# Kernel tuning notes

Measured on AMD Instinct MI355X. Metric: run time of the kernel, lower is better.

## Reference

```python
import jax, jax.numpy as jnp
import numpy as np

N_NODES = 50000
N_EDGES = 800000
D_NODE = 64
D_EDGE = 64


def setup_inputs() -> dict:
    key = jax.random.key(0)
    ks = jax.random.split(key, 6)
    node_scalars = jax.random.normal(ks[0], (N_NODES, D_NODE), dtype=jnp.float32)
    edge_feats = jax.random.normal(ks[1], (N_EDGES, D_EDGE), dtype=jnp.float32)
    src_idxs = jax.random.randint(ks[2], (N_EDGES,), 0, N_NODES, dtype=jnp.int32)
    dst_idxs = jax.random.randint(ks[3], (N_EDGES,), 0, N_NODES, dtype=jnp.int32)
    in_dim = 2 * D_NODE + D_EDGE  # 192
    # He-ish init for the MLP weights
    W1 = jax.random.normal(ks[4], (in_dim, D_EDGE), dtype=jnp.float32) / np.sqrt(in_dim)
    b1 = jnp.zeros((D_EDGE,), dtype=jnp.float32)
    W2 = jax.random.normal(ks[5], (D_EDGE, D_EDGE), dtype=jnp.float32) / np.sqrt(D_EDGE)
    b2 = jnp.zeros((D_EDGE,), dtype=jnp.float32)
    ln_gamma = jnp.ones((D_EDGE,), dtype=jnp.float32)
    ln_beta = jnp.zeros((D_EDGE,), dtype=jnp.float32)
    return {
        "node_scalars": node_scalars,
        "edge_feats": edge_feats,
        "src_idxs": src_idxs,
        "dst_idxs": dst_idxs,
        "W1": W1,
        "b1": b1,
        "W2": W2,
        "b2": b2,
        "ln_gamma": ln_gamma,
        "ln_beta": ln_beta,
    }


def _layer_norm(x, gamma, beta, eps=1e-5):
    mu = jnp.mean(x, axis=-1, keepdims=True)
    var = jnp.mean(jnp.square(x - mu), axis=-1, keepdims=True)
    return (x - mu) * jax.lax.rsqrt(var + eps) * gamma + beta


def reference(node_scalars, edge_feats, src_idxs, dst_idxs, W1, b1, W2, b2, ln_gamma, ln_beta):
    # gather endpoint node features per edge and concat with edge feats -> [E, 2*Dn + De]
    mlp_in = jnp.concatenate(
        [node_scalars[src_idxs], node_scalars[dst_idxs], edge_feats], axis=-1
    )
    h = jax.nn.silu(mlp_in @ W1 + b1)
    h = jax.nn.silu(h @ W2 + b2)
    return _layer_norm(edge_feats + h, ln_gamma, ln_beta)
```

## Files before the change

kernel.cpp:

```cpp
#include <hip/hip_runtime.h>

#define NE 800000
#define NN 50000
#define D  64
#define K1 192
#define AST 200
#define WSW_ELEMS (K1 * D + D * D)

typedef __bf16 bf16x4v __attribute__((ext_vector_type(4)));
typedef __bf16 bf16x8  __attribute__((ext_vector_type(8)));
typedef float  f32x4   __attribute__((ext_vector_type(4)));

__global__ void prep_all(const float* __restrict__ W1,
                         const float* __restrict__ W2,
                         const float* __restrict__ nodes,
                         __bf16* __restrict__ ws, int do_nodes) {
  const int b = blockIdx.x;
  if (b < 64) {
    int i = b * 256 + threadIdx.x;
    if (i < K1 * D) {
      int k = i >> 6, n = i & 63;
      ws[n * K1 + k] = (__bf16)W1[i];
    } else {
      int j = i - K1 * D;
      int k = j >> 6, n = j & 63;
      ws[K1 * D + n * D + k] = (__bf16)W2[j];
    }
  } else if (do_nodes) {
    __bf16* nb = ws + WSW_ELEMS;
    const int nvec = NN * D / 4;
    for (int v = (b - 64) * 256 + threadIdx.x; v < nvec; v += 2048 * 256) {
      f32x4 x = *(const f32x4*)(nodes + (size_t)v * 4);
      bf16x4v y;
      #pragma unroll
      for (int j = 0; j < 4; ++j) y[j] = (__bf16)x[j];
      *(bf16x4v*)(nb + (size_t)v * 4) = y;
    }
  }
}

__device__ __forceinline__ void wave_lds_fence() {
  __asm__ volatile("s_waitcnt lgkmcnt(0)" ::: "memory");
}

__device__ __forceinline__ float silu(float x) {
  return x * __builtin_amdgcn_rcpf(1.f + __expf(-x));
}

template <int MODE>
__global__ __launch_bounds__(256, 3)
void edge_kernel(const float* __restrict__ nodes, const float* __restrict__ ef,
                 const int* __restrict__ srci, const int* __restrict__ dsti,
                 const float* __restrict__ W1, const float* __restrict__ b1,
                 const float* __restrict__ W2, const float* __restrict__ b2,
                 const float* __restrict__ gmm, const float* __restrict__ bta,
                 const __bf16* __restrict__ wsw, float* __restrict__ out) {
  __shared__ __align__(16) __bf16 w1t[64 * AST];
  __shared__ __align__(16) __bf16 atile_all[4][16 * AST];
  __shared__ float sb1[64], sb2[64], sg[64], sbt[64];

  const int tid = threadIdx.x;
  const int wave = tid >> 6, lane = tid & 63;
  const int quad = lane >> 4, m16 = lane & 15;

  if (MODE >= 1) {
    const uint2* s1 = (const uint2*)wsw;
    for (int c = tid; c < 3072; c += 256) {
      int n = c / 48, kc = c - n * 48;
      *(uint2*)&w1t[n * AST + kc * 4] = s1[c];
    }
  } else {
    for (int i = tid; i < K1 * D; i += 256) {
      int k = i >> 6, n = i & 63;
      w1t[n * AST + k] = (__bf16)W1[i];
    }
  }
  if (tid < 64)       sb1[tid]       = b1[tid];
  else if (tid < 128) sb2[tid - 64]  = b2[tid - 64];
  else if (tid < 192) sg[tid - 128]  = gmm[tid - 128];
  else                sbt[tid - 192] = bta[tid - 192];

  bf16x8 w2f[2][4];
  if (MODE >= 1) {
    const __bf16* w2t = wsw + K1 * D;
    #pragma unroll
    for (int ki = 0; ki < 2; ++ki)
      #pragma unroll
      for (int nt = 0; nt < 4; ++nt)
        w2f[ki][nt] = *(const bf16x8*)&w2t[(nt * 16 + m16) * 64 + ki * 32 + quad * 8];
  } else {
    #pragma unroll
    for (int ki = 0; ki < 2; ++ki)
      #pragma unroll
      for (int nt = 0; nt < 4; ++nt) {
        const int n = nt * 16 + m16;
        #pragma unroll
        for (int j = 0; j < 8; ++j)
          w2f[ki][nt][j] = (__bf16)W2[(ki * 32 + quad * 8 + j) * 64 + n];
      }
  }
  __syncthreads();

  __bf16* At = atile_all[wave];
  float*  Af = (float*)At;

  const __bf16* nb = (MODE == 2) ? (wsw + WSW_ELEMS) : nullptr;

  #pragma unroll 1
  for (int t = 0; t < 4; ++t) {
    const int base = blockIdx.x * 256 + wave * 64 + t * 16;

    int si[4], di[4];
    #pragma unroll
    for (int i = 0; i < 4; ++i) {
      si[i] = srci[base + i * 4 + quad];
      di[i] = dsti[base + i * 4 + quad];
    }
    #pragma unroll
    for (int i = 0; i < 4; ++i) {
      const int row = i * 4 + quad;
      f32x4 ev = *(const f32x4*)(ef + (size_t)(base + row) * D + m16 * 4);
      bf16x4v sb, db, eb;
      if (MODE == 2) {
        sb = *(const bf16x4v*)(nb + (size_t)si[i] * D + m16 * 4);
        db = *(const bf16x4v*)(nb + (size_t)di[i] * D + m16 * 4);
      } else {
        f32x4 sv = *(const f32x4*)(nodes + (size_t)si[i] * D + m16 * 4);
        f32x4 dv = *(const f32x4*)(nodes + (size_t)di[i] * D + m16 * 4);
        #pragma unroll
        for (int j = 0; j < 4; ++j) { sb[j] = (__bf16)sv[j]; db[j] = (__bf16)dv[j]; }
      }
      #pragma unroll
      for (int j = 0; j < 4; ++j) eb[j] = (__bf16)ev[j];
      *(bf16x4v*)&At[row * AST +       m16 * 4] = sb;
      *(bf16x4v*)&At[row * AST +  64 + m16 * 4] = db;
      *(bf16x4v*)&At[row * AST + 128 + m16 * 4] = eb;
    }
    wave_lds_fence();

    f32x4 acc[4] = {};
    #pragma unroll
    for (int ki = 0; ki < 6; ++ki) {
      bf16x8 a = *(const bf16x8*)&At[m16 * AST + ki * 32 + quad * 8];
      #pragma unroll
      for (int nt = 0; nt < 4; ++nt) {
        bf16x8 bfv = *(const bf16x8*)&w1t[(nt * 16 + m16) * AST + ki * 32 + quad * 8];
        acc[nt] = __builtin_amdgcn_mfma_f32_16x16x32_bf16(a, bfv, acc[nt], 0, 0, 0);
      }
    }

    #pragma unroll
    for (int nt = 0; nt < 4; ++nt) {
      const int c = nt * 16 + m16;
      const float bb = sb1[c];
      #pragma unroll
      for (int r = 0; r < 4; ++r)
        At[(quad * 4 + r) * AST + c] = (__bf16)silu(acc[nt][r] + bb);
    }
    wave_lds_fence();

    f32x4 acc2[4] = {};
    #pragma unroll
    for (int ki = 0; ki < 2; ++ki) {
      bf16x8 a = *(const bf16x8*)&At[m16 * AST + ki * 32 + quad * 8];
      #pragma unroll
      for (int nt = 0; nt < 4; ++nt)
        acc2[nt] = __builtin_amdgcn_mfma_f32_16x16x32_bf16(a, w2f[ki][nt], acc2[nt], 0, 0, 0);
    }

    #pragma unroll
    for (int r = 0; r < 4; ++r) {
      const int row = quad * 4 + r;
      float x[4];
      float sum = 0.f;
      #pragma unroll
      for (int nt = 0; nt < 4; ++nt) {
        const int c = nt * 16 + m16;
        float h = silu(acc2[nt][r] + sb2[c]);
        float efv = (float)At[row * AST + 128 + c];
        x[nt] = efv + h;
        sum += x[nt];
      }
      float sq = x[0] * x[0] + x[1] * x[1] + x[2] * x[2] + x[3] * x[3];
      #pragma unroll
      for (int off = 1; off < 16; off <<= 1) {
        sum += __shfl_xor(sum, off);
        sq  += __shfl_xor(sq, off);
      }
      const float mean = sum * (1.f / 64.f);
      const float var  = sq * (1.f / 64.f) - mean * mean;
      const float rstd = rsqrtf(var + 1e-5f);
      #pragma unroll
      for (int nt = 0; nt < 4; ++nt) {
        const int c = nt * 16 + m16;
        Af[row * (AST / 2) + c] = (x[nt] - mean) * rstd * sg[c] + sbt[c];
      }
    }
    wave_lds_fence();

    #pragma unroll
    for (int i = 0; i < 4; ++i) {
      const int row = i * 4 + quad;
      f32x4 ov = *(const f32x4*)&Af[row * (AST / 2) + m16 * 4];
      *(f32x4*)(out + (size_t)(base + row) * D + m16 * 4) = ov;
    }
    wave_lds_fence();
  }
}

extern "C" void kernel_launch(void* const* d_in, const int* in_sizes, int n_in,
                              void* d_out, int out_size, void* d_ws, size_t ws_size,
                              hipStream_t stream) {
  const float* nodes = (const float*)d_in[0];
  const float* ef    = (const float*)d_in[1];
  const int*   srci  = (const int*)d_in[2];
  const int*   dsti  = (const int*)d_in[3];
  const float* W1    = (const float*)d_in[4];
  const float* b1    = (const float*)d_in[5];
  const float* W2    = (const float*)d_in[6];
  const float* b2    = (const float*)d_in[7];
  const float* gmm   = (const float*)d_in[8];
  const float* bta   = (const float*)d_in[9];
  float* out = (float*)d_out;

  const int blocks = NE / 256;
  const size_t WS_W = (size_t)WSW_ELEMS * 2;
  const size_t WS_FULL = WS_W + (size_t)NN * D * 2;

  if (ws_size >= WS_FULL) {
    prep_all<<<64 + 2048, 256, 0, stream>>>(W1, W2, nodes, (__bf16*)d_ws, 1);
    edge_kernel<2><<<blocks, 256, 0, stream>>>(
        nodes, ef, srci, dsti, W1, b1, W2, b2, gmm, bta,
        (const __bf16*)d_ws, out);
  } else if (ws_size >= WS_W) {
    prep_all<<<64, 256, 0, stream>>>(W1, W2, nodes, (__bf16*)d_ws, 0);
    edge_kernel<1><<<blocks, 256, 0, stream>>>(
        nodes, ef, srci, dsti, W1, b1, W2, b2, gmm, bta,
        (const __bf16*)d_ws, out);
  } else {
    edge_kernel<0><<<blocks, 256, 0, stream>>>(
        nodes, ef, srci, dsti, W1, b1, W2, b2, gmm, bta, nullptr, out);
  }
}
```

Baseline: 398.1 us.

## Software-pipeline gathers across tiles and store output directly from registers

Prefetches the next tile's edge indices, node gathers and edge features into registers while the current tile's first GEMM runs, with the loop fully unrolled and sched barriers pinning the loads in place. This aims to hide gather latency behind MFMA work. It also drops the LDS staging of the LayerNorm output and writes scalar floats straight to global memory. That removes an LDS round trip but makes the stores strided 4-byte writes instead of 16-byte vectors. The register prefetch buffers raise register pressure, and occupancy is pinned to exactly 3 waves per EU.

```diff
diff --git a/kernel.cpp b/kernel.cpp
--- a/kernel.cpp
+++ b/kernel.cpp
@@ -48,7 +48,8 @@
 }
 
 template <int MODE>
-__global__ __launch_bounds__(256, 3)
+__global__ __launch_bounds__(256)
+__attribute__((amdgpu_waves_per_eu(3, 3)))
 void edge_kernel(const float* __restrict__ nodes, const float* __restrict__ ef,
                  const int* __restrict__ srci, const int* __restrict__ dsti,
                  const float* __restrict__ W1, const float* __restrict__ b1,
@@ -102,39 +103,60 @@
   __syncthreads();
 
   __bf16* At = atile_all[wave];
-  float*  Af = (float*)At;
 
   const __bf16* nb = (MODE == 2) ? (wsw + WSW_ELEMS) : nullptr;
-
-  #pragma unroll 1
+  const int wbase = blockIdx.x * 256 + wave * 64;
+
+  bf16x4v sb[4], db[4];
+  f32x4 svf[4], dvf[4];
+  f32x4 ev[4];
+  int si[4], di[4];
+
+  #pragma unroll
+  for (int i = 0; i < 4; ++i) {
+    si[i] = srci[wbase + i * 4 + quad];
+    di[i] = dsti[wbase + i * 4 + quad];
+  }
+  #pragma unroll
+  for (int i = 0; i < 4; ++i) {
+    const int row = i * 4 + quad;
+    if (MODE == 2) {
+      sb[i] = *(const bf16x4v*)(nb + (size_t)si[i] * D + m16 * 4);
+      db[i] = *(const bf16x4v*)(nb + (size_t)di[i] * D + m16 * 4);
+    } else {
+      svf[i] = *(const f32x4*)(nodes + (size_t)si[i] * D + m16 * 4);
+      dvf[i] = *(const f32x4*)(nodes + (size_t)di[i] * D + m16 * 4);
+    }
+    ev[i] = *(const f32x4*)(ef + (size_t)(wbase + row) * D + m16 * 4);
+  }
+
+  #pragma unroll
   for (int t = 0; t < 4; ++t) {
-    const int base = blockIdx.x * 256 + wave * 64 + t * 16;
-
-    int si[4], di[4];
-    #pragma unroll
-    for (int i = 0; i < 4; ++i) {
-      si[i] = srci[base + i * 4 + quad];
-      di[i] = dsti[base + i * 4 + quad];
-    }
+    const int base = wbase + t * 16;
+
     #pragma unroll
     for (int i = 0; i < 4; ++i) {
       const int row = i * 4 + quad;
-      f32x4 ev = *(const f32x4*)(ef + (size_t)(base + row) * D + m16 * 4);
-      bf16x4v sb, db, eb;
+      bf16x4v s_, d_, e_;
       if (MODE == 2) {
-        sb = *(const bf16x4v*)(nb + (size_t)si[i] * D + m16 * 4);
-        db = *(const bf16x4v*)(nb + (size_t)di[i] * D + m16 * 4);
+        s_ = sb[i]; d_ = db[i];
       } else {
-        f32x4 sv = *(const f32x4*)(nodes + (size_t)si[i] * D + m16 * 4);
-        f32x4 dv = *(const f32x4*)(nodes + (size_t)di[i] * D + m16 * 4);
         #pragma unroll
-        for (int j = 0; j < 4; ++j) { sb[j] = (__bf16)sv[j]; db[j] = (__bf16)dv[j]; }
-      }
-      #pragma unroll
-      for (int j = 0; j < 4; ++j) eb[j] = (__bf16)ev[j];
-      *(bf16x4v*)&At[row * AST +       m16 * 4] = sb;
-      *(bf16x4v*)&At[row * AST +  64 + m16 * 4] = db;
-      *(bf16x4v*)&At[row * AST + 128 + m16 * 4] = eb;
+        for (int j = 0; j < 4; ++j) { s_[j] = (__bf16)svf[i][j]; d_[j] = (__bf16)dvf[i][j]; }
+      }
+      #pragma unroll
+      for (int j = 0; j < 4; ++j) e_[j] = (__bf16)ev[i][j];
+      *(bf16x4v*)&At[row * AST +       m16 * 4] = s_;
+      *(bf16x4v*)&At[row * AST +  64 + m16 * 4] = d_;
+      *(bf16x4v*)&At[row * AST + 128 + m16 * 4] = e_;
+    }
+
+    if (t < 3) {
+      #pragma unroll
+      for (int i = 0; i < 4; ++i) {
+        si[i] = srci[base + 16 + i * 4 + quad];
+        di[i] = dsti[base + 16 + i * 4 + quad];
+      }
     }
     wave_lds_fence();
 
@@ -147,6 +169,23 @@
         bf16x8 bfv = *(const bf16x8*)&w1t[(nt * 16 + m16) * AST + ki * 32 + quad * 8];
         acc[nt] = __builtin_amdgcn_mfma_f32_16x16x32_bf16(a, bfv, acc[nt], 0, 0, 0);
       }
+    }
+
+    if (t < 3) {
+      __builtin_amdgcn_sched_barrier(0);
+      #pragma unroll
+      for (int i = 0; i < 4; ++i) {
+        const int row = i * 4 + quad;
+        if (MODE == 2) {
+          sb[i] = *(const bf16x4v*)(nb + (size_t)si[i] * D + m16 * 4);
+          db[i] = *(const bf16x4v*)(nb + (size_t)di[i] * D + m16 * 4);
+        } else {
+          svf[i] = *(const f32x4*)(nodes + (size_t)si[i] * D + m16 * 4);
+          dvf[i] = *(const f32x4*)(nodes + (size_t)di[i] * D + m16 * 4);
+        }
+        ev[i] = *(const f32x4*)(ef + (size_t)(base + 16 + row) * D + m16 * 4);
+      }
+      __builtin_amdgcn_sched_barrier(0);
     }
 
     #pragma unroll
@@ -193,16 +232,8 @@
       #pragma unroll
       for (int nt = 0; nt < 4; ++nt) {
         const int c = nt * 16 + m16;
-        Af[row * (AST / 2) + c] = (x[nt] - mean) * rstd * sg[c] + sbt[c];
-      }
-    }
-    wave_lds_fence();
-
-    #pragma unroll
-    for (int i = 0; i < 4; ++i) {
-      const int row = i * 4 + quad;
-      f32x4 ov = *(const f32x4*)&Af[row * (AST / 2) + m16 * 4];
-      *(f32x4*)(out + (size_t)(base + row) * D + m16 * 4) = ov;
+        out[(size_t)(base + row) * D + c] = (x[nt] - mean) * rstd * sg[c] + sbt[c];
+      }
     }
     wave_lds_fence();
   }
```

Result: no change. 393.0 us (-1.3%).
